# Kernel tuning notes

Hardware: AMD Instinct MI355X
Metric: run time of the kernel (lower is better)

The kernel has to match this reference:

```python
import jax, jax.numpy as jnp
import numpy as np

B, IMG, C = 128, 128, 3
NP = 8                      # n_patches per side
PS = IMG // NP              # patch size = 16
IN_D = C * PS * PS          # 768
E, NH, L, A = 768, 12, 12, 256
HS = E // NH                # 64
T = NP * NP + 1             # 65 tokens (cls + patches)
LN_EPS = 1e-5


def _pos_emb(seq_len, d):
    i = np.arange(seq_len, dtype=np.float64)[:, None]
    j = np.arange(d, dtype=np.float64)[None, :]
    even = np.sin(i / 10000 ** (j / d))
    odd = np.cos(i / 10000 ** ((j - 1) / d))
    return jnp.asarray(np.where(j % 2 == 0, even, odd), dtype=jnp.float32)


def setup_inputs() -> dict:
    key = jax.random.key(0)
    ks = jax.random.split(key, 16)
    s_e = 1.0 / np.sqrt(E)
    s_in = 1.0 / np.sqrt(IN_D)
    s_4e = 1.0 / np.sqrt(4 * E)
    return {
        "images": jax.random.normal(ks[0], (B, IMG, IMG, C), jnp.float32),
        "lin_w": jax.random.normal(ks[1], (IN_D, E), jnp.float32) * s_in,
        "cls_tok": jax.random.uniform(ks[2], (1, E), jnp.float32),
        "pos_emb": _pos_emb(T, E),
        "Wq": jax.random.normal(ks[3], (L, E, E), jnp.float32) * s_e,
        "Wk": jax.random.normal(ks[4], (L, E, E), jnp.float32) * s_e,
        "Wv": jax.random.normal(ks[5], (L, E, E), jnp.float32) * s_e,
        "Wo": jax.random.normal(ks[6], (L, E, E), jnp.float32) * s_e,
        "bo": jnp.zeros((L, E), jnp.float32),
        "ln1g": jnp.ones((L, E), jnp.float32),
        "ln1b": jnp.zeros((L, E), jnp.float32),
        "ln2g": jnp.ones((L, E), jnp.float32),
        "ln2b": jnp.zeros((L, E), jnp.float32),
        "W1": jax.random.normal(ks[7], (L, E, 4 * E), jnp.float32) * s_e,
        "b1": jnp.zeros((L, 4 * E), jnp.float32),
        "W2": jax.random.normal(ks[8], (L, 4 * E, E), jnp.float32) * s_4e,
        "b2": jnp.zeros((L, E), jnp.float32),
        "head_w": jax.random.normal(ks[9], (E, A), jnp.float32) * s_e,
        "head_b": jnp.zeros((A,), jnp.float32),
    }


def _layernorm(x, g, b):
    mu = jnp.mean(x, axis=-1, keepdims=True)
    var = jnp.var(x, axis=-1, keepdims=True)
    return (x - mu) * jax.lax.rsqrt(var + LN_EPS) * g + b


def _vit_forward(images, lin_w, cls_tok, pos_emb, Wq, Wk, Wv, Wo, bo,
                 ln1g, ln1b, ln2g, ln2b, W1, b1, W2, b2, head_w, head_b):
    n = images.shape[0]
    # patches: 'b (h p1) (w p2) c -> b (h w) (p1 p2 c)'
    p = images.reshape(n, NP, PS, NP, PS, C)
    patches = p.transpose(0, 1, 3, 2, 4, 5).reshape(n, NP * NP, IN_D)
    x = patches @ lin_w                                   # [B, 64, E]
    x = jnp.concatenate([jnp.broadcast_to(cls_tok, (n, 1, E)), x], axis=1)
    x = x + pos_emb[None]                                 # [B, T, E]

    scale = E ** (-0.5)  # NOTE: original scales by n_embd, not head_size

    def block(x, params):
        wq, wk, wv, wo_, bo_, g1, be1, g2, be2, w1, bb1, w2, bb2 = params
        h = _layernorm(x, g1, be1)
        q = (h @ wq).reshape(n, T, NH, HS)
        k = (h @ wk).reshape(n, T, NH, HS)
        v = (h @ wv).reshape(n, T, NH, HS)
        wei = jnp.einsum('bthd,bshd->bhts', q, k) * scale
        wei = jax.nn.softmax(wei, axis=-1)
        attn = jnp.einsum('bhts,bshd->bthd', wei, v).reshape(n, T, E)
        x = x + attn @ wo_ + bo_
        h2 = _layernorm(x, g2, be2)
        x = x + jax.nn.relu(h2 @ w1 + bb1) @ w2 + bb2
        return x, None

    x, _ = jax.lax.scan(block, x,
                        (Wq, Wk, Wv, Wo, bo, ln1g, ln1b, ln2g, ln2b,
                         W1, b1, W2, b2))
    cls = x[:, 0]                                          # [B, E]
    logits = jax.nn.softmax(cls @ head_w + head_b, axis=-1)  # model ends in Softmax
    return logits


def reference(images, lin_w, cls_tok, pos_emb, Wq, Wk, Wv, Wo, bo,
              ln1g, ln1b, ln2g, ln2b, W1, b1, W2, b2, head_w, head_b):
    return _vit_forward(images, lin_w, cls_tok, pos_emb, Wq, Wk, Wv, Wo, bo,
                        ln1g, ln1b, ln2g, ln2b, W1, b1, W2, b2, head_w, head_b)
```

## Files before the change

### kernel.cpp

```cpp
#include <hip/hip_runtime.h>
#include <cstdint>
#include <cstddef>


typedef __bf16 bf16x8 __attribute__((ext_vector_type(8)));
typedef float  f32x4  __attribute__((ext_vector_type(4)));

#define DEVINL __device__ __forceinline__

DEVINL uint16_t f2bf(float f){
  union U{float f; uint32_t i;} v; v.f=f; uint32_t u=v.i;
  return (uint16_t)((u + 0x7fffu + ((u>>16)&1u)) >> 16);
}

DEVINL void gl_lds16(const void* g, void* l){
  __builtin_amdgcn_global_load_lds((const __attribute__((address_space(1))) void*)g,
                                   (__attribute__((address_space(3))) void*)l, 16, 0, 0);
}

__global__ __launch_bounds__(256) void patchify_k(const float* __restrict__ img,
                                                  uint16_t* __restrict__ out){
  int i = blockIdx.x*256 + threadIdx.x;
  int m  = i / 768, kk = i - m*768;
  int b  = m >> 6,  t  = m & 63;
  int py = t >> 3,  px = t & 7;
  int r  = kk / 48, rem = kk - r*48;
  size_t src = ((size_t)(b*128 + py*16 + r)*128 + px*16)*3 + rem;
  out[i] = f2bf(img[src]);
}

DEVINL void tile_transpose(const float* __restrict__ src, uint16_t* __restrict__ dst,
                           int R, int C, int ti, int tj, int tid){
  __shared__ uint16_t tile[32][33];
  int tx = tid & 31, ty = tid >> 5;
  int r0 = ti*32, c0 = tj*32;
  #pragma unroll
  for (int i=0;i<4;++i)
    tile[ty+i*8][tx] = f2bf(src[(size_t)(r0+ty+i*8)*C + c0 + tx]);
  __syncthreads();
  #pragma unroll
  for (int i=0;i<4;++i)
    dst[(size_t)(c0+ty+i*8)*R + r0 + tx] = tile[tx][ty+i*8];
}

__global__ __launch_bounds__(256) void transpose_cvt_k(const float* __restrict__ src,
                                                       uint16_t* __restrict__ dst, int R, int C){
  tile_transpose(src, dst, R, C, blockIdx.y, blockIdx.x, threadIdx.x);
}

__global__ __launch_bounds__(256) void prep_layer_k(
    const float* __restrict__ Wq, const float* __restrict__ Wk,
    const float* __restrict__ Wv, const float* __restrict__ Wo,
    const float* __restrict__ W1, const float* __restrict__ W2,
    uint16_t* __restrict__ wbuf){
  int idx = blockIdx.x;
  const float* src; uint16_t* dst; int R, C, ti, tj;
  if (idx < 2304){
    int m = idx / 576, t = idx - m*576; ti = t/24; tj = t - ti*24; R=768; C=768;
    src = (m==0)?Wq:(m==1)?Wk:(m==2)?Wv:Wo;
    dst = wbuf + (size_t)m*589824;
  } else if (idx < 4608){
    int t = idx - 2304; ti = t/96; tj = t - ti*96; R=768; C=3072;
    src = W1; dst = wbuf + 2359296;
  } else {
    int t = idx - 4608; ti = t/24; tj = t - ti*24; R=3072; C=768;
    src = W2; dst = wbuf + 4718592;
  }
  tile_transpose(src, dst, R, C, ti, tj, threadIdx.x);
}

__global__ __launch_bounds__(256) void cls_init_k(const float* __restrict__ ct,
                                                  const float* __restrict__ pos,
                                                  float* __restrict__ X){
  int b = blockIdx.x, tid = threadIdx.x;
  for (int e = tid; e < 768; e += 256)
    X[(size_t)b*65*768 + e] = ct[e] + pos[e];
}

template<int MODE>
__global__ __launch_bounds__(256) void ln_k(const float* __restrict__ Xin,
                                            float* __restrict__ Xout,
                                            const float* __restrict__ Pa,
                                            const float* __restrict__ bias2,
                                            uint16_t* __restrict__ H,
                                            const float* __restrict__ g,
                                            const float* __restrict__ b){
  const int row  = blockIdx.x*4 + (threadIdx.x>>6);
  const int lane = threadIdx.x & 63;
  const size_t ro = (size_t)row*768;
  const float4* xr = (const float4*)(Xin + ro);
  float4 v[3];
  #pragma unroll
  for (int j=0;j<3;++j) v[j] = xr[lane + j*64];
  if constexpr (MODE==1){
    const float4* pr = (const float4*)(Pa + ro);
    #pragma unroll
    for (int j=0;j<3;++j){
      float4 p = pr[lane + j*64];
      v[j].x += p.x; v[j].y += p.y; v[j].z += p.z; v[j].w += p.w;
    }
  } else if constexpr (MODE==2){
    const float4* pr = (const float4*)(Pa + ro);
    const float4* br = (const float4*)(bias2);
    #pragma unroll
    for (int j=0;j<3;++j){
      float4 p = pr[lane + j*64];
      float4 bb = br[lane + j*64];
      v[j].x += p.x + bb.x; v[j].y += p.y + bb.y;
      v[j].z += p.z + bb.z; v[j].w += p.w + bb.w;
    }
  }
  if constexpr (MODE!=0){
    float4* xo = (float4*)(Xout + ro);
    #pragma unroll
    for (int j=0;j<3;++j) xo[lane + j*64] = v[j];
  }
  float s = 0.f;
  #pragma unroll
  for (int j=0;j<3;++j) s += v[j].x + v[j].y + v[j].z + v[j].w;
  #pragma unroll
  for (int off=32; off; off>>=1) s += __shfl_xor(s, off);
  const float mu = s * (1.f/768.f);
  float q = 0.f;
  #pragma unroll
  for (int j=0;j<3;++j){
    float dx=v[j].x-mu, dy=v[j].y-mu, dz=v[j].z-mu, dw=v[j].w-mu;
    q += dx*dx + dy*dy + dz*dz + dw*dw;
  }
  #pragma unroll
  for (int off=32; off; off>>=1) q += __shfl_xor(q, off);
  const float rs = rsqrtf(q*(1.f/768.f) + 1e-5f);
  const float4* gr = (const float4*)g;
  const float4* br2 = (const float4*)b;
  ushort4* hr = (ushort4*)(H + ro);
  #pragma unroll
  for (int j=0;j<3;++j){
    float4 gv = gr[lane + j*64];
    float4 bv = br2[lane + j*64];
    ushort4 o;
    o.x = f2bf((v[j].x-mu)*rs*gv.x + bv.x);
    o.y = f2bf((v[j].y-mu)*rs*gv.y + bv.y);
    o.z = f2bf((v[j].z-mu)*rs*gv.z + bv.z);
    o.w = f2bf((v[j].w-mu)*rs*gv.w + bv.w);
    hr[lane + j*64] = o;
  }
}

enum { EP_BF16=0, EP_RES=1, EP_RELU=2, EP_EMB=3, EP_OUTF32=4 };

template<int MODE, int BN>
__global__ __launch_bounds__(256) void gemm_bt_k(
    const uint16_t* __restrict__ A, const uint16_t* __restrict__ Bt,
    int M, int N, int K, int strideB, long long strideO,
    const float* __restrict__ bias, float* __restrict__ X,
    uint16_t* __restrict__ Obf, const float* __restrict__ pos,
    float* __restrict__ Pout)
{
  constexpr int WN = BN/2;
  constexpr int NF = WN/16;
  constexpr int BLOADS = BN/64;
  __shared__ __align__(16) uint16_t sA[3][128*32];
  __shared__ __align__(16) uint16_t sB[3][BN*32];
  const int tid = threadIdx.x;
  const int wid = tid>>6, lane = tid&63;
  const int nx = gridDim.x;
  const int nwg = nx*gridDim.y;
  int idx = blockIdx.y*nx + blockIdx.x;
  int q8 = nwg>>3, r8 = nwg&7, xcd = idx&7, off = idx>>3;
  int swz = (xcd<r8 ? xcd*(q8+1) : r8*(q8+1) + (xcd-r8)*q8) + off;
  const int bn = (swz % nx)*BN, bm = (swz / nx)*128;
  const int z = blockIdx.z;
  const uint16_t* Bz = Bt + (size_t)z*strideB;
  const int wr = wid>>1, wc = wid&1;
  const int frow = lane&15, g = lane>>4;
  int srA[2], scA[2];
  #pragma unroll
  for (int rr=0; rr<2; ++rr){
    int G = rr*256 + tid;
    srA[rr] = G>>2; scA[rr] = ((G&3) - (G>>3)) & 3;
  }
  int srB[BLOADS], scB[BLOADS];
  #pragma unroll
  for (int rr=0; rr<BLOADS; ++rr){
    int G = rr*256 + tid;
    srB[rr] = G>>2; scB[rr] = ((G&3) - (G>>3)) & 3;
  }
  const int rsw = (frow>>1)&3;
  f32x4 acc[4][NF] = {};
  const int nt = K>>5;

  auto stage = [&](char* dA, char* dB, int k0){
    #pragma unroll
    for (int rr=0; rr<2; ++rr)
      gl_lds16(A + (size_t)(bm+srA[rr])*K + k0 + scA[rr]*8, dA + (rr*256 + wid*64)*16);
    #pragma unroll
    for (int rr=0; rr<BLOADS; ++rr)
      gl_lds16(Bz + (size_t)(bn+srB[rr])*K + k0 + scB[rr]*8, dB + (rr*256 + wid*64)*16);
  };

  char *cA=(char*)sA[0], *nA=(char*)sA[1], *fA=(char*)sA[2];
  char *cB=(char*)sB[0], *nB=(char*)sB[1], *fB=(char*)sB[2];
  stage(cA, cB, 0);
  stage(nA, nB, 32);

  for (int t = 0; t < nt; ++t){
    if (t+2 < nt){
      stage(fA, fB, (t+2)<<5);
      if constexpr (BLOADS==1) asm volatile("s_waitcnt vmcnt(6)" ::: "memory");
      else                     asm volatile("s_waitcnt vmcnt(8)" ::: "memory");
    } else if (t+1 < nt){
      if constexpr (BLOADS==1) asm volatile("s_waitcnt vmcnt(3)" ::: "memory");
      else                     asm volatile("s_waitcnt vmcnt(4)" ::: "memory");
    } else {
      asm volatile("s_waitcnt vmcnt(0)" ::: "memory");
    }
    __builtin_amdgcn_s_barrier();
    bf16x8 a[4], b[NF];
    #pragma unroll
    for (int m=0;m<4;++m)
      a[m] = *(const bf16x8*)(cA + (wr*64+m*16+frow)*64 + (((g+rsw)&3)<<4));
    #pragma unroll
    for (int n=0;n<NF;++n)
      b[n] = *(const bf16x8*)(cB + (wc*WN+n*16+frow)*64 + (((g+rsw)&3)<<4));
    #pragma unroll
    for (int m=0;m<4;++m)
      #pragma unroll
      for (int n=0;n<NF;++n)
        acc[m][n] = __builtin_amdgcn_mfma_f32_16x16x32_bf16(a[m], b[n], acc[m][n], 0,0,0);
    __builtin_amdgcn_s_barrier();
    char* t1=cA; cA=nA; nA=fA; fA=t1;
    char* t2=cB; cB=nB; nB=fB; fB=t2;
  }

  uint16_t* Oz = Obf ? Obf + (size_t)z*(size_t)strideO : nullptr;
  #pragma unroll
  for (int m=0;m<4;++m){
    int gr0 = bm + wr*64 + m*16 + (lane>>4)*4;
    #pragma unroll
    for (int n=0;n<NF;++n){
      int gc = bn + wc*WN + n*16 + (lane&15);
      #pragma unroll
      for (int r=0;r<4;++r){
        int grow = gr0 + r;
        float vsum = acc[m][n][r];
        if constexpr (MODE==EP_BF16){
          Oz[(size_t)grow*N + gc] = f2bf(vsum);
        } else if constexpr (MODE==EP_RES){
          X[(size_t)grow*N + gc] += vsum + bias[gc];
        } else if constexpr (MODE==EP_RELU){
          float u = vsum + bias[gc];
          Oz[(size_t)grow*N + gc] = f2bf(u > 0.f ? u : 0.f);
        } else if constexpr (MODE==EP_OUTF32){
          Pout[(size_t)grow*N + gc] = vsum;
        } else {
          int t2i = grow & 63, bb = grow >> 6;
          X[((size_t)bb*65 + 1 + t2i)*768 + gc] = vsum + pos[(size_t)(t2i+1)*768 + gc];
        }
      }
    }
  }
}

template<int MODE, int SK>
__global__ __launch_bounds__(512) void gemm2m_k(
    const uint16_t* __restrict__ A, const uint16_t* __restrict__ Bt,
    int M, int N, int K, int strideB, long long strideO,
    const float* __restrict__ bias, float* __restrict__ X,
    uint16_t* __restrict__ Obf, float* __restrict__ P1)
{
  __shared__ __align__(16) uint16_t sA[2][256*32];
  __shared__ __align__(16) uint16_t sB[2][128*32];
  const int tid = threadIdx.x;
  const int wid = tid>>6, lane = tid&63;
  const int nx = gridDim.x;
  const int nwg = nx*gridDim.y;
  int idx = blockIdx.y*nx + blockIdx.x;
  int q8 = nwg>>3, r8 = nwg&7, xcd = idx&7, off = idx>>3;
  int swz = (xcd<r8 ? xcd*(q8+1) : r8*(q8+1) + (xcd-r8)*q8) + off;
  const int bn = (swz % nx)*128, bm = (swz / nx)*256;
  const int z = blockIdx.z;
  const uint16_t* Bz = (SK==1) ? Bt + (size_t)z*strideB : Bt;
  const int kbase = (SK==1) ? 0 : z*(K/SK);
  const int KS = (SK==1) ? K : K/SK;
  const int wr = wid>>1, wc = wid&1;
  const int frow = lane&15, g = lane>>4;
  int srA[2], scA[2];
  #pragma unroll
  for (int rr=0; rr<2; ++rr){
    int G = rr*512 + tid;
    srA[rr] = G>>2; scA[rr] = ((G&3) - (G>>3)) & 3;
  }
  const int srB = tid>>2, scB = ((tid&3) - (tid>>3)) & 3;
  const int rsw = (frow>>1)&3;
  f32x4 acc[4][4] = {};
  const int nt = KS>>5;

  auto stage = [&](int bsel, int k0){
    char* dA = (char*)sA[bsel]; char* dB = (char*)sB[bsel];
    #pragma unroll
    for (int rr=0; rr<2; ++rr)
      gl_lds16(A + (size_t)(bm+srA[rr])*K + kbase + k0 + scA[rr]*8,
               dA + (rr*512 + wid*64)*16);
    gl_lds16(Bz + (size_t)(bn+srB)*K + kbase + k0 + scB*8, dB + (wid*64)*16);
  };

  stage(0, 0);
  int buf = 0;
  for (int t = 0; t < nt; ++t){
    if (t+1 < nt){
      stage(buf^1, (t+1)<<5);
      asm volatile("s_waitcnt vmcnt(3)" ::: "memory");
    } else {
      asm volatile("s_waitcnt vmcnt(0)" ::: "memory");
    }
    __builtin_amdgcn_s_barrier();
    const char* sAc = (const char*)sA[buf];
    const char* sBc = (const char*)sB[buf];
    bf16x8 a[4], b[4];
    #pragma unroll
    for (int m=0;m<4;++m)
      a[m] = *(const bf16x8*)(sAc + (wr*64+m*16+frow)*64 + (((g+rsw)&3)<<4));
    #pragma unroll
    for (int n=0;n<4;++n)
      b[n] = *(const bf16x8*)(sBc + (wc*64+n*16+frow)*64 + (((g+rsw)&3)<<4));
    __builtin_amdgcn_s_setprio(1);
    #pragma unroll
    for (int m=0;m<4;++m)
      #pragma unroll
      for (int n=0;n<4;++n)
        acc[m][n] = __builtin_amdgcn_mfma_f32_16x16x32_bf16(a[m], b[n], acc[m][n], 0,0,0);
    __builtin_amdgcn_s_setprio(0);
    __builtin_amdgcn_s_barrier();
    buf ^= 1;
  }

  uint16_t* Oz = Obf ? Obf + (size_t)z*(size_t)strideO : nullptr;
  #pragma unroll
  for (int m=0;m<4;++m){
    int gr0 = bm + wr*64 + m*16 + (lane>>4)*4;
    #pragma unroll
    for (int n=0;n<4;++n){
      int gc = bn + wc*64 + n*16 + (lane&15);
      #pragma unroll
      for (int r=0;r<4;++r){
        int grow = gr0 + r;
        if (grow < M){
          float vsum = acc[m][n][r];
          if constexpr (MODE==EP_BF16){
            Oz[(size_t)grow*N + gc] = f2bf(vsum);
          } else if constexpr (MODE==EP_RES){
            if constexpr (SK==1){
              X[(size_t)grow*N + gc] += vsum + bias[gc];
            } else {
              if (z==0) X[(size_t)grow*N + gc] += vsum + bias[gc];
              else      P1[(size_t)grow*N + gc] = vsum;
            }
          } else if constexpr (MODE==EP_RELU){
            float u = vsum + bias[gc];
            Oz[(size_t)grow*N + gc] = f2bf(u > 0.f ? u : 0.f);
          }
        }
      }
    }
  }
}

__global__ __launch_bounds__(320) void attn_mfma_k(const uint16_t* __restrict__ q,
    const uint16_t* __restrict__ k, const uint16_t* __restrict__ v,
    uint16_t* __restrict__ o)
{
  __shared__ __align__(16) uint16_t P_lds[80][104];
  __shared__ __align__(16) uint16_t Vt[64][104];
  const int bh = blockIdx.x; const int b = bh / 12, hd = bh - b*12;
  const int tid = threadIdx.x;
  const int m = tid>>6;
  const int lane = tid&63;
  const int g = lane>>4, c = lane&15;
  const size_t base = (size_t)b*65*768 + (size_t)hd*64;

  for (int i = tid; i < 80*16; i += 320) P_lds[i>>4][80 + (i&15)] = 0;
  for (int i = tid; i < 64*32; i += 320) Vt[i>>5][64 + (i&31)] = 0;
  __syncthreads();
  for (int j = tid; j < 520; j += 320){
    int key = j >> 3, dc = j & 7;
    union { bf16x8 v8; uint16_t u[8]; } gv;
    gv.v8 = *(const bf16x8*)&v[base + (size_t)key*768 + dc*8];
    #pragma unroll
    for (int e = 0; e < 8; ++e) Vt[dc*8 + e][key] = gv.u[e];
  }

  bf16x8 bk[5][2];
  #pragma unroll
  for (int n=0;n<5;++n)
    #pragma unroll
    for (int kk=0;kk<2;++kk)
      bk[n][kk] = *(const bf16x8*)&k[base + (size_t)(n*16 + c)*768 + kk*32 + g*8];

  bf16x8 aq[2];
  #pragma unroll
  for (int kk=0;kk<2;++kk)
    aq[kk] = *(const bf16x8*)&q[base + (size_t)(m*16 + c)*768 + kk*32 + g*8];
  f32x4 sacc[5] = {};
  #pragma unroll
  for (int kk=0;kk<2;++kk)
    #pragma unroll
    for (int n=0;n<5;++n)
      sacc[n] = __builtin_amdgcn_mfma_f32_16x16x32_bf16(aq[kk], bk[n][kk], sacc[n], 0,0,0);

  const float scale = 0.03608439182435161f;
  #pragma unroll
  for (int r=0;r<4;++r){
    float val[5]; float mx = -3.0e38f;
    #pragma unroll
    for (int n=0;n<5;++n){
      val[n] = (n*16 + c) < 65 ? sacc[n][r]*scale : -3.0e38f;
      mx = fmaxf(mx, val[n]);
    }
    #pragma unroll
    for (int off=1; off<16; off<<=1) mx = fmaxf(mx, __shfl_xor(mx, off));
    float p[5], sum = 0.f;
    #pragma unroll
    for (int n=0;n<5;++n){
      p[n] = (n*16 + c) < 65 ? __expf(val[n]-mx) : 0.f;
      sum += p[n];
    }
    #pragma unroll
    for (int off=1; off<16; off<<=1) sum += __shfl_xor(sum, off);
    float rinv = 1.f / sum;
    int row = m*16 + g*4 + r;
    #pragma unroll
    for (int n=0;n<5;++n) P_lds[row][n*16 + c] = f2bf(p[n]*rinv);
  }
  __syncthreads();

  bf16x8 vb[4][3];
  #pragma unroll
  for (int n=0;n<4;++n)
    #pragma unroll
    for (int kk=0;kk<3;++kk)
      vb[n][kk] = *(const bf16x8*)&Vt[n*16 + c][kk*32 + g*8];
  f32x4 oacc[4] = {};
  #pragma unroll
  for (int kk=0;kk<3;++kk){
    bf16x8 pa = *(const bf16x8*)&P_lds[m*16 + c][kk*32 + g*8];
    #pragma unroll
    for (int n=0;n<4;++n)
      oacc[n] = __builtin_amdgcn_mfma_f32_16x16x32_bf16(pa, vb[n][kk], oacc[n], 0,0,0);
  }
  #pragma unroll
  for (int r=0;r<4;++r){
    int row = m*16 + g*4 + r;
    if (row < 65){
      #pragma unroll
      for (int n=0;n<4;++n)
        o[base + (size_t)row*768 + n*16 + c] = f2bf(oacc[n][r]);
    }
  }
}

__global__ __launch_bounds__(256) void head_k(const float* __restrict__ X,
    const float* __restrict__ P1,
    const float* __restrict__ W, const float* __restrict__ bias,
    float* __restrict__ out){
  int b = blockIdx.x, a = threadIdx.x;
  const size_t ro = (size_t)b*65*768;
  const float* xr = X + ro;
  const float* p1 = P1 + ro;
  float acc = bias[a];
  for (int kk=0; kk<768; ++kk)
    acc += (xr[kk]+p1[kk])*W[(size_t)kk*256 + a];
  int wid = a>>6, lane = a&63;
  __shared__ float red[4];
  float mx = acc;
  #pragma unroll
  for (int off=32; off; off>>=1) mx = fmaxf(mx, __shfl_xor(mx, off));
  if (lane==0) red[wid]=mx;
  __syncthreads();
  mx = fmaxf(fmaxf(red[0],red[1]), fmaxf(red[2],red[3]));
  float e = __expf(acc-mx);
  float s = e;
  #pragma unroll
  for (int off=32; off; off>>=1) s += __shfl_xor(s, off);
  __syncthreads();
  if (lane==0) red[wid]=s;
  __syncthreads();
  s = red[0]+red[1]+red[2]+red[3];
  out[(size_t)b*256 + a] = e/s;
}

extern "C" void kernel_launch(void* const* d_in, const int* in_sizes, int n_in,
                              void* d_out, int out_size, void* d_ws, size_t ws_size,
                              hipStream_t stream)
{
  const float* images = (const float*)d_in[0];
  const float* lin_w  = (const float*)d_in[1];
  const float* cls_tok= (const float*)d_in[2];
  const float* pos    = (const float*)d_in[3];
  const float* Wq = (const float*)d_in[4];
  const float* Wk = (const float*)d_in[5];
  const float* Wv = (const float*)d_in[6];
  const float* Wo = (const float*)d_in[7];
  const float* bo = (const float*)d_in[8];
  const float* ln1g=(const float*)d_in[9];
  const float* ln1b=(const float*)d_in[10];
  const float* ln2g=(const float*)d_in[11];
  const float* ln2b=(const float*)d_in[12];
  const float* W1 = (const float*)d_in[13];
  const float* b1 = (const float*)d_in[14];
  const float* W2 = (const float*)d_in[15];
  const float* b2 = (const float*)d_in[16];
  const float* hw = (const float*)d_in[17];
  const float* hb = (const float*)d_in[18];

  char* ws = (char*)d_ws;
  float*    x    = (float*)   (ws + 0);
  uint16_t* attn = (uint16_t*)(ws + 25559040);
  float*    P1   = (float*)   (ws + 25559040);
  uint16_t* qkv  = (uint16_t*)(ws + 38338560);
  uint16_t* h    = (uint16_t*)(ws + 76677120);
  uint16_t* mid  = (uint16_t*)(ws + 89456640);
  float*    woP  = (float*)   (ws + 89456640);
  uint16_t* wbuf = (uint16_t*)(ws + 140574720);
  uint16_t* lwt  = (uint16_t*)(ws + 154730496);

  patchify_k<<<24576,256,0,stream>>>(images, mid);
  transpose_cvt_k<<<dim3(24,24),256,0,stream>>>(lin_w, lwt, 768, 768);
  gemm_bt_k<EP_EMB,128><<<dim3(6,64,1),256,0,stream>>>(mid, lwt, 8192,768,768, 0,0,
                                                   nullptr, x, nullptr, pos, nullptr);
  cls_init_k<<<128,256,0,stream>>>(cls_tok, pos, x);

  for (int l=0;l<12;++l){
    prep_layer_k<<<6912,256,0,stream>>>(Wq+(size_t)l*589824, Wk+(size_t)l*589824,
                                        Wv+(size_t)l*589824, Wo+(size_t)l*589824,
                                        W1+(size_t)l*2359296, W2+(size_t)l*2359296, wbuf);
    if (l==0)
      ln_k<0><<<2080,256,0,stream>>>(x, nullptr, nullptr, nullptr, h, ln1g, ln1b);
    else
      ln_k<1><<<2080,256,0,stream>>>(x, x, P1, nullptr, h,
                                     ln1g+(size_t)l*768, ln1b+(size_t)l*768);
    gemm2m_k<EP_BF16,1><<<dim3(6,33,3),512,0,stream>>>(h, wbuf, 8320,768,768,
                                                       589824, 6389760LL,
                                                       nullptr, nullptr, qkv, nullptr);
    attn_mfma_k<<<1536,320,0,stream>>>(qkv, qkv+6389760, qkv+12779520, attn);
    gemm_bt_k<EP_OUTF32,128><<<dim3(6,65,1),256,0,stream>>>(attn, wbuf+1769472,
                                                     8320,768,768, 0,0,
                                                     nullptr, nullptr, nullptr, nullptr, woP);
    ln_k<2><<<2080,256,0,stream>>>(x, x, woP, bo+(size_t)l*768, h,
                                   ln2g+(size_t)l*768, ln2b+(size_t)l*768);
    gemm2m_k<EP_RELU,1><<<dim3(24,33,1),512,0,stream>>>(h, wbuf+2359296, 8320,3072,768,
                                                        0,0, b1+(size_t)l*3072, nullptr, mid, nullptr);
    gemm2m_k<EP_RES,2><<<dim3(6,33,2),512,0,stream>>>(mid, wbuf+4718592, 8320,768,3072,
                                                      0,0, b2+(size_t)l*768, x, nullptr, P1);
  }
  head_k<<<128,256,0,stream>>>(x, P1, hw, hb, (float*)d_out);
}
```

Measured before the change: 3.114 ms.

## Add 256x256 ping-pong GEMM for fused QKV and FC1, interleave QKV layout

Introduces a new 512-thread GEMM kernel with 256x256 output tiles, double-buffered direct global-to-LDS loads with a swizzled layout, split A/B staging across two half-phases, s_setprio around the MFMA bursts, and an XCD-aware block remap. The QKV projection now runs as a single N=2304 GEMM that writes an interleaved row layout instead of three z-sliced outputs, and attention is updated to read Q/K/V at stride 2304. FC1 with ReLU also moves to the new kernel. The goal is more operand reuse per LDS byte and better load/compute overlap. The cost is heavy register pressure from 32 accumulator tiles, and fewer workgroups (297 for QKV, 396 for FC1), which can leave the GPU under-filled.

```diff
diff --git a/kernel.cpp b/kernel.cpp
--- a/kernel.cpp
+++ b/kernel.cpp
@@ -365,8 +365,133 @@
   }
 }
 
-__global__ __launch_bounds__(320) void attn_mfma_k(const uint16_t* __restrict__ q,
-    const uint16_t* __restrict__ k, const uint16_t* __restrict__ v,
+template<int MODE>
+__global__ __launch_bounds__(512) void gemm8p_k(
+    const uint16_t* __restrict__ A, const uint16_t* __restrict__ Bt,
+    int M, int N, int K,
+    const float* __restrict__ bias, uint16_t* __restrict__ Obf)
+{
+  __shared__ uint16_t sA[2][256][64];
+  __shared__ uint16_t sB[2][256][64];
+  const int tid = threadIdx.x;
+  const int wid = tid>>6, lane = tid&63;
+  const int nx = gridDim.x;
+  const int nwg = nx*gridDim.y;
+  int idx = blockIdx.y*nx + blockIdx.x;
+  int q8 = nwg>>3, r8 = nwg&7, xcd = idx&7, off = idx>>3;
+  int swz = (xcd<r8 ? xcd*(q8+1) : r8*(q8+1) + (xcd-r8)*q8) + off;
+  const int bn = (swz % nx)*256, bm = (swz / nx)*256;
+  const int NT = K>>6;
+  const int wr = wid>>2, wc = wid&3;
+  const int frow = lane&15, g = lane>>4;
+
+  bf16x8 a[4][2], b[4][2];
+  f32x4 acc[8][4] = {};
+
+  auto stA = [&](int bs, int hf, int kt){
+    #pragma unroll
+    for (int rr=0; rr<2; ++rr){
+      int G = rr*512 + tid;
+      int row = G>>3, slot = G&7;
+      int chunk = (slot - row) & 7;
+      gl_lds16(A + (size_t)(bm + hf*128 + row)*K + kt*64 + chunk*8,
+               (char*)sA + ((size_t)bs*2048 + hf*1024 + rr*512 + wid*64)*16);
+    }
+  };
+  auto stB = [&](int bs, int hf, int kt){
+    #pragma unroll
+    for (int rr=0; rr<2; ++rr){
+      int G = rr*512 + tid;
+      int row = G>>3, slot = G&7;
+      int chunk = (slot - row) & 7;
+      gl_lds16(Bt + (size_t)(bn + hf*128 + row)*K + kt*64 + chunk*8,
+               (char*)sB + ((size_t)bs*2048 + hf*1024 + rr*512 + wid*64)*16);
+    }
+  };
+  auto rdA = [&](int bs, int mh){
+    #pragma unroll
+    for (int mm=0; mm<4; ++mm)
+      #pragma unroll
+      for (int ks=0; ks<2; ++ks){
+        int row = wr*128 + (mh*4+mm)*16 + frow;
+        int slot = (ks*4 + g + frow) & 7;
+        a[mm][ks] = *(const bf16x8*)&sA[bs][row][slot*8];
+      }
+  };
+  auto rdB = [&](int bs){
+    #pragma unroll
+    for (int nn=0; nn<4; ++nn)
+      #pragma unroll
+      for (int ks=0; ks<2; ++ks){
+        int row = wc*64 + nn*16 + frow;
+        int slot = (ks*4 + g + frow) & 7;
+        b[nn][ks] = *(const bf16x8*)&sB[bs][row][slot*8];
+      }
+  };
+
+#define BAR8() __builtin_amdgcn_s_barrier()
+#define MFMA32(MLO) do{                                                       \
+    __builtin_amdgcn_s_setprio(1);                                            \
+    _Pragma("unroll") for (int mm=0; mm<4; ++mm)                              \
+    _Pragma("unroll") for (int nn=0; nn<4; ++nn)                              \
+    _Pragma("unroll") for (int ks=0; ks<2; ++ks)                              \
+      acc[(MLO)+mm][nn] = __builtin_amdgcn_mfma_f32_16x16x32_bf16(            \
+          a[mm][ks], b[nn][ks], acc[(MLO)+mm][nn], 0,0,0);                    \
+    __builtin_amdgcn_s_setprio(0); }while(0)
+
+  stB(0,0,0); stB(0,1,0); stA(0,0,0); stA(0,1,0);
+  if (NT > 1){
+    stB(1,0,1); stB(1,1,1);
+    asm volatile("s_waitcnt vmcnt(4)" ::: "memory");
+  } else {
+    asm volatile("s_waitcnt vmcnt(0)" ::: "memory");
+  }
+  BAR8();
+
+  for (int t = 0; t < NT; ++t){
+    const int p = t & 1;
+    rdA(p,0); rdB(p);
+    if (t+1 < NT){ stA(p^1,0,t+1); stA(p^1,1,t+1); }
+    BAR8();
+    MFMA32(0);
+    BAR8();
+    rdA(p,1);
+    if (t+2 < NT){ stB(p,0,t+2); stB(p,1,t+2); }
+    BAR8();
+    MFMA32(4);
+    if (t+1 < NT){
+      if (t+2 < NT) asm volatile("s_waitcnt vmcnt(4)" ::: "memory");
+      else          asm volatile("s_waitcnt vmcnt(0)" ::: "memory");
+    }
+    BAR8();
+  }
+
+  #pragma unroll
+  for (int mm=0; mm<8; ++mm){
+    int gr0 = bm + wr*128 + mm*16 + g*4;
+    #pragma unroll
+    for (int nn=0; nn<4; ++nn){
+      int gc = bn + wc*64 + nn*16 + frow;
+      #pragma unroll
+      for (int r=0;r<4;++r){
+        int grow = gr0 + r;
+        if (grow < M){
+          float vsum = acc[mm][nn][r];
+          if constexpr (MODE==EP_BF16){
+            Obf[(size_t)grow*N + gc] = f2bf(vsum);
+          } else {
+            float u = vsum + bias[gc];
+            Obf[(size_t)grow*N + gc] = f2bf(u > 0.f ? u : 0.f);
+          }
+        }
+      }
+    }
+  }
+#undef BAR8
+#undef MFMA32
+}
+
+__global__ __launch_bounds__(320) void attn_mfma_k(const uint16_t* __restrict__ qkv,
     uint16_t* __restrict__ o)
 {
   __shared__ __align__(16) uint16_t P_lds[80][104];
@@ -376,7 +501,8 @@
   const int m = tid>>6;
   const int lane = tid&63;
   const int g = lane>>4, c = lane&15;
-  const size_t base = (size_t)b*65*768 + (size_t)hd*64;
+  const size_t base  = (size_t)b*65*2304 + (size_t)hd*64;
+  const size_t obase = (size_t)b*65*768  + (size_t)hd*64;
 
   for (int i = tid; i < 80*16; i += 320) P_lds[i>>4][80 + (i&15)] = 0;
   for (int i = tid; i < 64*32; i += 320) Vt[i>>5][64 + (i&31)] = 0;
@@ -384,7 +510,7 @@
   for (int j = tid; j < 520; j += 320){
     int key = j >> 3, dc = j & 7;
     union { bf16x8 v8; uint16_t u[8]; } gv;
-    gv.v8 = *(const bf16x8*)&v[base + (size_t)key*768 + dc*8];
+    gv.v8 = *(const bf16x8*)&qkv[base + 1536 + (size_t)key*2304 + dc*8];
     #pragma unroll
     for (int e = 0; e < 8; ++e) Vt[dc*8 + e][key] = gv.u[e];
   }
@@ -394,12 +520,12 @@
   for (int n=0;n<5;++n)
     #pragma unroll
     for (int kk=0;kk<2;++kk)
-      bk[n][kk] = *(const bf16x8*)&k[base + (size_t)(n*16 + c)*768 + kk*32 + g*8];
+      bk[n][kk] = *(const bf16x8*)&qkv[base + 768 + (size_t)(n*16 + c)*2304 + kk*32 + g*8];
 
   bf16x8 aq[2];
   #pragma unroll
   for (int kk=0;kk<2;++kk)
-    aq[kk] = *(const bf16x8*)&q[base + (size_t)(m*16 + c)*768 + kk*32 + g*8];
+    aq[kk] = *(const bf16x8*)&qkv[base + (size_t)(m*16 + c)*2304 + kk*32 + g*8];
   f32x4 sacc[5] = {};
   #pragma unroll
   for (int kk=0;kk<2;++kk)
@@ -453,7 +579,7 @@
     if (row < 65){
       #pragma unroll
       for (int n=0;n<4;++n)
-        o[base + (size_t)row*768 + n*16 + c] = f2bf(oacc[n][r]);
+        o[obase + (size_t)row*768 + n*16 + c] = f2bf(oacc[n][r]);
     }
   }
 }
@@ -538,17 +664,16 @@
     else
       ln_k<1><<<2080,256,0,stream>>>(x, x, P1, nullptr, h,
                                      ln1g+(size_t)l*768, ln1b+(size_t)l*768);
-    gemm2m_k<EP_BF16,1><<<dim3(6,33,3),512,0,stream>>>(h, wbuf, 8320,768,768,
-                                                       589824, 6389760LL,
-                                                       nullptr, nullptr, qkv, nullptr);
-    attn_mfma_k<<<1536,320,0,stream>>>(qkv, qkv+6389760, qkv+12779520, attn);
+    gemm8p_k<EP_BF16><<<dim3(9,33,1),512,0,stream>>>(h, wbuf, 8320,2304,768,
+                                                     nullptr, qkv);
+    attn_mfma_k<<<1536,320,0,stream>>>(qkv, attn);
     gemm_bt_k<EP_OUTF32,128><<<dim3(6,65,1),256,0,stream>>>(attn, wbuf+1769472,
                                                      8320,768,768, 0,0,
                                                      nullptr, nullptr, nullptr, nullptr, woP);
     ln_k<2><<<2080,256,0,stream>>>(x, x, woP, bo+(size_t)l*768, h,
                                    ln2g+(size_t)l*768, ln2b+(size_t)l*768);
-    gemm2m_k<EP_RELU,1><<<dim3(24,33,1),512,0,stream>>>(h, wbuf+2359296, 8320,3072,768,
-                                                        0,0, b1+(size_t)l*3072, nullptr, mid, nullptr);
+    gemm8p_k<EP_RELU><<<dim3(12,33,1),512,0,stream>>>(h, wbuf+2359296, 8320,3072,768,
+                                                      b1+(size_t)l*3072, mid);
     gemm2m_k<EP_RES,2><<<dim3(6,33,2),512,0,stream>>>(mid, wbuf+4718592, 8320,768,3072,
                                                       0,0, b2+(size_t)l*768, x, nullptr, P1);
   }
```

New measurement: 3.287 ms. 5.5% more time.
